# Kernel optimization log

Hardware: AMD Instinct MI355X
Metric: run time of the kernel (lower is better)

Reference implementation:

```python
import jax, jax.numpy as jnp
import numpy as np


def setup_inputs() -> dict:
    key = jax.random.key(0)
    k1, k2 = jax.random.split(key)
    B, K, S = 262144, 32, 30
    sparse_code = jax.random.normal(k1, (B, K), dtype=jnp.float32)
    dictionary = jax.random.normal(k2, (S * S, K), dtype=jnp.float32)
    return {"sparse_code": sparse_code, "dictionary": dictionary, "image_size": S}


def reference(sparse_code, dictionary, image_size):
    # matmul(dictionary, sparse_code.T).T == sparse_code @ dictionary.T -> [B, S*S]
    samples = jnp.einsum("bk,dk->bd", sparse_code, dictionary)
    B = samples.shape[0]
    img = samples.reshape(B, image_size, image_size)
    # Serpentine unrolling: flip every odd row (rows 1,3,...,image_size-1)
    img = img.at[:, 1::2, :].set(img[:, 1::2, ::-1])
    return img[:, None, :, :]  # [B, 1, S, S]
```

## Files before the change

### kernel.cpp

```cpp
#include <hip/hip_runtime.h>
#include <hip/hip_bf16.h>


typedef __attribute__((ext_vector_type(8))) short bf16x8;
typedef __attribute__((ext_vector_type(4))) float f32x4;

constexpr int KD    = 32;
constexpr int DDIM  = 900;
constexpr int SDIM  = 30;
constexpr int NCHT  = 57;
constexpr int TROWS = 16;
constexpr int TILES = 8;
constexpr int RPB   = TROWS * TILES;
constexpr int STGW  = 464;

__device__ __forceinline__ int serp_src(int d) {
    int r = d / SDIM, c = d - r * SDIM;
    return (r & 1) ? (r * SDIM + (SDIM - 1 - c)) : d;
}

__device__ __forceinline__ short f2bf(float x) {
    __hip_bfloat16 h = __float2bfloat16(x);
    short u; __builtin_memcpy(&u, &h, 2); return u;
}

__device__ __forceinline__ void barrier_lds() {
    __builtin_amdgcn_sched_barrier(0);
    asm volatile("s_waitcnt lgkmcnt(0)" ::: "memory");
    __builtin_amdgcn_sched_barrier(0);
    __builtin_amdgcn_s_barrier();
    __builtin_amdgcn_sched_barrier(0);
}

__global__ __launch_bounds__(256) void mfma_decode(
    const float* __restrict__ sc,
    const float* __restrict__ dict,
    float* __restrict__ out,
    int B)
{
    __shared__ alignas(16) float stg[TROWS * STGW];

    const int t    = threadIdx.x;
    const int lane = t & 63;
    const int wid  = t >> 6;

    bf16x8 df[15];
    #pragma unroll
    for (int j = 0; j < 15; ++j) {
        int ch = wid + 4 * j; if (ch > NCHT - 1) ch = NCHT - 1;
        int d  = ch * 16 + (lane & 15);
        int dd = (d < DDIM) ? d : (DDIM - 1);
        const float* p = dict + (size_t)serp_src(dd) * KD + ((lane >> 4) << 3);
        const float4 f0 = *reinterpret_cast<const float4*>(p);
        const float4 f1 = *reinterpret_cast<const float4*>(p + 4);
        bf16x8 a;
        a[0] = f2bf(f0.x); a[1] = f2bf(f0.y); a[2] = f2bf(f0.z); a[3] = f2bf(f0.w);
        a[4] = f2bf(f1.x); a[5] = f2bf(f1.y); a[6] = f2bf(f1.z); a[7] = f2bf(f1.w);
        df[j] = a;
    }

    const int brow = lane & 15;
    const int k0   = (lane >> 4) << 3;
    const int dloc = (lane >> 4) << 2;
    const long long b0 = (long long)blockIdx.x * RPB;

    const float* ap0 = sc + (size_t)(b0 + brow) * KD + k0;
    float4 pf0 = *reinterpret_cast<const float4*>(ap0);
    float4 pf1 = *reinterpret_cast<const float4*>(ap0 + 4);

    for (int tile = 0; tile < TILES; ++tile) {
        const long long rowg = b0 + (long long)tile * TROWS;

        bf16x8 bb;
        bb[0] = f2bf(pf0.x); bb[1] = f2bf(pf0.y); bb[2] = f2bf(pf0.z); bb[3] = f2bf(pf0.w);
        bb[4] = f2bf(pf1.x); bb[5] = f2bf(pf1.y); bb[6] = f2bf(pf1.z); bb[7] = f2bf(pf1.w);

        if (tile + 1 < TILES) {
            const float* apn = sc + (size_t)(rowg + TROWS + brow) * KD + k0;
            pf0 = *reinterpret_cast<const float4*>(apn);
            pf1 = *reinterpret_cast<const float4*>(apn + 4);
        }

        float* __restrict__ tbase = out + (size_t)rowg * DDIM;

        #pragma unroll
        for (int P = 0; P < 2; ++P) {
            #pragma unroll
            for (int j = 0; j < 15; ++j) {
                const int ch = wid + 4 * j;
                const bool mine = (P == 0) ? (ch < 28) : (ch >= 28 && ch < NCHT);
                if (mine) {
                    f32x4 z = {0.f, 0.f, 0.f, 0.f};
                    f32x4 acc = __builtin_amdgcn_mfma_f32_16x16x32_bf16(df[j], bb, z, 0, 0, 0);
                    const int dl = ch * 16 + dloc - P * 448;
                    *reinterpret_cast<f32x4*>(&stg[brow * STGW + dl]) = acc;
                }
            }
            barrier_lds();

            if (P == 0) {
                #pragma unroll
                for (int i = 0; i < 7; ++i) {
                    const int idx = i * 256 + t;
                    const int row = idx / 112;
                    const int c4  = idx - row * 112;
                    f32x4 v = *reinterpret_cast<const f32x4*>(&stg[row * STGW + c4 * 4]);
                    *reinterpret_cast<f32x4*>(tbase + (size_t)row * DDIM + c4 * 4) = v;
                }
            } else {
                #pragma unroll
                for (int i = 0; i < 8; ++i) {
                    const int idx = i * 256 + t;
                    if (idx < 1808) {
                        const int row = idx / 113;
                        const int c4  = idx - row * 113;
                        f32x4 v = *reinterpret_cast<const f32x4*>(&stg[row * STGW + c4 * 4]);
                        *reinterpret_cast<f32x4*>(tbase + (size_t)row * DDIM + 448 + c4 * 4) = v;
                    }
                }
            }
            barrier_lds();
        }
    }
}

extern "C" void kernel_launch(void* const* d_in, const int* in_sizes, int n_in,
                              void* d_out, int out_size, void* d_ws, size_t ws_size,
                              hipStream_t stream) {
    const float* sc   = (const float*)d_in[0];
    const float* dict = (const float*)d_in[1];
    float* out        = (float*)d_out;

    const int B = in_sizes[0] / KD;

    mfma_decode<<<dim3((unsigned)(B / RPB)), 256, 0, stream>>>(sc, dict, out, B);
}
```

Baseline: 219.2 us.

## Stage full 16x900 tile in LDS and store output as one contiguous block

Replaces the two-phase staging (two 448/452-column halves with padded stride) with a single LDS buffer holding the whole 16-row by 900-column tile in output layout. All MFMA results are written before one barrier, and the copy-out becomes a flat contiguous stream of 14 float4 stores per thread plus a tail. This removes one barrier pair per tile and the index division math, and makes global stores fully contiguous. In exchange LDS use roughly doubles to about 57.6KB, which may reduce blocks per CU, and the unpadded 900 stride may cause LDS bank conflicts on the MFMA writes.

```diff
diff --git a/kernel.cpp b/kernel.cpp
--- a/kernel.cpp
+++ b/kernel.cpp
@@ -12,7 +12,6 @@
 constexpr int TROWS = 16;
 constexpr int TILES = 8;
 constexpr int RPB   = TROWS * TILES;
-constexpr int STGW  = 464;
 
 __device__ __forceinline__ int serp_src(int d) {
     int r = d / SDIM, c = d - r * SDIM;
@@ -38,7 +37,7 @@
     float* __restrict__ out,
     int B)
 {
-    __shared__ alignas(16) float stg[TROWS * STGW];
+    __shared__ alignas(16) float stg[TROWS * DDIM];
 
     const int t    = threadIdx.x;
     const int lane = t & 63;
@@ -81,46 +80,35 @@
             pf1 = *reinterpret_cast<const float4*>(apn + 4);
         }
 
-        float* __restrict__ tbase = out + (size_t)rowg * DDIM;
-
         #pragma unroll
-        for (int P = 0; P < 2; ++P) {
-            #pragma unroll
-            for (int j = 0; j < 15; ++j) {
-                const int ch = wid + 4 * j;
-                const bool mine = (P == 0) ? (ch < 28) : (ch >= 28 && ch < NCHT);
-                if (mine) {
-                    f32x4 z = {0.f, 0.f, 0.f, 0.f};
-                    f32x4 acc = __builtin_amdgcn_mfma_f32_16x16x32_bf16(df[j], bb, z, 0, 0, 0);
-                    const int dl = ch * 16 + dloc - P * 448;
-                    *reinterpret_cast<f32x4*>(&stg[brow * STGW + dl]) = acc;
+        for (int j = 0; j < 15; ++j) {
+            const int ch = wid + 4 * j;
+            if (ch < NCHT) {
+                f32x4 z = {0.f, 0.f, 0.f, 0.f};
+                f32x4 acc = __builtin_amdgcn_mfma_f32_16x16x32_bf16(df[j], bb, z, 0, 0, 0);
+                if (ch != 56) {
+                    *reinterpret_cast<f32x4*>(&stg[brow * DDIM + ch * 16 + dloc]) = acc;
+                } else if (dloc == 0) {
+                    *reinterpret_cast<f32x4*>(&stg[brow * DDIM + 896]) = acc;
                 }
             }
-            barrier_lds();
+        }
+        barrier_lds();
 
-            if (P == 0) {
-                #pragma unroll
-                for (int i = 0; i < 7; ++i) {
-                    const int idx = i * 256 + t;
-                    const int row = idx / 112;
-                    const int c4  = idx - row * 112;
-                    f32x4 v = *reinterpret_cast<const f32x4*>(&stg[row * STGW + c4 * 4]);
-                    *reinterpret_cast<f32x4*>(tbase + (size_t)row * DDIM + c4 * 4) = v;
-                }
-            } else {
-                #pragma unroll
-                for (int i = 0; i < 8; ++i) {
-                    const int idx = i * 256 + t;
-                    if (idx < 1808) {
-                        const int row = idx / 113;
-                        const int c4  = idx - row * 113;
-                        f32x4 v = *reinterpret_cast<const f32x4*>(&stg[row * STGW + c4 * 4]);
-                        *reinterpret_cast<f32x4*>(tbase + (size_t)row * DDIM + 448 + c4 * 4) = v;
-                    }
-                }
-            }
-            barrier_lds();
+        float* __restrict__ tbase = out + (size_t)rowg * DDIM;
+        const int base = t * 4;
+        #pragma unroll
+        for (int i = 0; i < 14; ++i) {
+            const int o = i * 1024 + base;
+            f32x4 v = *reinterpret_cast<const f32x4*>(&stg[o]);
+            *reinterpret_cast<f32x4*>(tbase + o) = v;
         }
+        if (t < 16) {
+            const int o = 14336 + base;
+            f32x4 v = *reinterpret_cast<const f32x4*>(&stg[o]);
+            *reinterpret_cast<f32x4*>(tbase + o) = v;
+        }
+        barrier_lds();
     }
 }
 
```

Result: faster. 203.3 us (-7.2%).
